# Kernel tuning notes

Hardware: AMD Instinct MI355X
Metric: run time of the kernel (lower is better)

The kernel has to match this reference:

```python
import jax, jax.numpy as jnp
import numpy as np

B, L, D = 4, 2048, 1024
H, DH = 16, 64  # heads, head dim (D = H*DH)


def setup_inputs() -> dict:
    key = jax.random.key(0)
    k1, k2, k3 = jax.random.split(key, 3)
    scale = D ** -0.5
    xin = jax.random.normal(k1, (B, L, D), dtype=jnp.float32)
    W_qkv = jax.random.normal(k2, (D, 3 * D), dtype=jnp.float32) * scale
    W_o = jax.random.normal(k3, (D, D), dtype=jnp.float32) * scale
    return {"xin": xin, "W_qkv": W_qkv, "W_o": W_o}


def reference(xin, W_qkv, W_o):
    b, Lq, _ = xin.shape
    # QKV projection: (b, L, 3D). NOTE: original torch code reshapes the
    # (b, L, 3D) buffer directly to (b, 3, H, L, DH) — a non-standard axis
    # interleave — which we replicate faithfully.
    QKV = (xin @ W_qkv).reshape(b, 3, H, Lq, DH)
    Q, K, V = QKV[:, 0], QKV[:, 1], QKV[:, 2]  # each (b, H, L, DH)
    scores = jnp.einsum("bhqd,bhkd->bhqk", Q, K) * (DH ** -0.5)
    attn = jax.nn.softmax(scores, axis=-1)  # dropout_prob=0.0 -> identity
    out = jnp.einsum("bhqk,bhkd->bhqd", attn, V)
    out = out.transpose(0, 2, 1, 3).reshape(b, Lq, H * DH)
    return out @ W_o
```

## Files before the change

### kernel.cpp

```cpp
#include <hip/hip_runtime.h>
#include <stdint.h>

typedef short short8 __attribute__((ext_vector_type(8)));
typedef float f32x4 __attribute__((ext_vector_type(4)));

#define LOG2E 1.44269504088896f
#define AS1 __attribute__((address_space(1)))
#define AS3 __attribute__((address_space(3)))

__device__ __forceinline__ float bfbits2f(unsigned short b) {
    unsigned u = ((unsigned)b) << 16;
    return __builtin_bit_cast(float, u);
}
__device__ __forceinline__ unsigned short f2bfbits(float f) {
    unsigned x = __builtin_bit_cast(unsigned, f);
    unsigned r = x + 0x7fffu + ((x >> 16) & 1u);
    return (unsigned short)(r >> 16);
}
__device__ __forceinline__ void unpack8(uint4 u, float4& f0, float4& f1) {
    f0.x = bfbits2f((unsigned short)(u.x & 0xffffu)); f0.y = bfbits2f((unsigned short)(u.x >> 16));
    f0.z = bfbits2f((unsigned short)(u.y & 0xffffu)); f0.w = bfbits2f((unsigned short)(u.y >> 16));
    f1.x = bfbits2f((unsigned short)(u.z & 0xffffu)); f1.y = bfbits2f((unsigned short)(u.z >> 16));
    f1.z = bfbits2f((unsigned short)(u.w & 0xffffu)); f1.w = bfbits2f((unsigned short)(u.w >> 16));
}
__device__ __forceinline__ unsigned pack2(float a, float b) {
    return (unsigned)f2bfbits(a) | ((unsigned)f2bfbits(b) << 16);
}
__device__ __forceinline__ float rsum16(float x) {
    x += __builtin_bit_cast(float, __builtin_amdgcn_mov_dpp(__builtin_bit_cast(int, x), 0x128, 0xf, 0xf, true));
    x += __builtin_bit_cast(float, __builtin_amdgcn_mov_dpp(__builtin_bit_cast(int, x), 0x124, 0xf, 0xf, true));
    x += __builtin_bit_cast(float, __builtin_amdgcn_mov_dpp(__builtin_bit_cast(int, x), 0x122, 0xf, 0xf, true));
    x += __builtin_bit_cast(float, __builtin_amdgcn_mov_dpp(__builtin_bit_cast(int, x), 0x121, 0xf, 0xf, true));
    return x;
}
__device__ __forceinline__ void glds16(const void* gp, void* lp) {
    __builtin_amdgcn_global_load_lds((const AS1 unsigned*)(uintptr_t)gp,
                                     (AS3 unsigned*)(unsigned)(uintptr_t)lp, 16, 0, 0);
}

__global__ __launch_bounds__(256) void xbf_k(const float* __restrict__ x,
                                             unsigned short* __restrict__ y) {
    int i = (blockIdx.x * 256 + threadIdx.x) * 4;
    float4 v = *(const float4*)(x + i);
    uint2 u;
    u.x = pack2(v.x, v.y);
    u.y = pack2(v.z, v.w);
    *(uint2*)(y + i) = u;
}

__global__ __launch_bounds__(256) void t32cvt_k(const float* __restrict__ src,
                                                unsigned short* __restrict__ dst,
                                                int R, int C) {
    __shared__ float tile[32][36];
    int t = threadIdx.x;
    int bx = blockIdx.x, by = blockIdx.y;
    int r = t >> 3, c0 = (t & 7) * 4;
    *(float4*)&tile[r][c0] = *(const float4*)(src + (size_t)(by * 32 + r) * C + bx * 32 + c0);
    __syncthreads();
    uint2 u;
    u.x = pack2(tile[c0 + 0][r], tile[c0 + 1][r]);
    u.y = pack2(tile[c0 + 2][r], tile[c0 + 3][r]);
    *(uint2*)(dst + (size_t)(bx * 32 + r) * R + by * 32 + c0) = u;
}

template <bool CF32>
__global__ __launch_bounds__(256) void gemm_k(const unsigned short* __restrict__ A,
                                              const unsigned short* __restrict__ Bt,
                                              void* __restrict__ Cv,
                                              int M, int N, int K) {
    __shared__ unsigned short sA[128 * 32];
    __shared__ unsigned short sB[128 * 32];
    int t = threadIdx.x;
    int wid = t >> 6, lane = t & 63;
    int wm = (wid >> 1) * 64, wn = (wid & 1) * 64;
    int lm = lane & 15, lq = lane >> 4;
    size_t m0 = (size_t)blockIdx.y * 128, n0 = (size_t)blockIdx.x * 128;
    int srow = t >> 2, scol = (t & 3) * 8;
    const unsigned short* ga0 = A + (m0 + srow) * K + scol;
    const unsigned short* ga1 = A + (m0 + 64 + srow) * K + scol;
    const unsigned short* gb0 = Bt + (n0 + srow) * K + scol;
    const unsigned short* gb1 = Bt + (n0 + 64 + srow) * K + scol;
    unsigned short* laA0 = &sA[wid * 512];
    unsigned short* laA1 = &sA[2048 + wid * 512];
    unsigned short* laB0 = &sB[wid * 512];
    unsigned short* laB1 = &sB[2048 + wid * 512];
    f32x4 acc[4][4] = {};
    for (int k0 = 0; k0 < K; k0 += 32) {
        __syncthreads();
        glds16(ga0 + k0, laA0);
        glds16(ga1 + k0, laA1);
        glds16(gb0 + k0, laB0);
        glds16(gb1 + k0, laB1);
        __syncthreads();
        short8 af[4], bfr[4];
        #pragma unroll
        for (int i = 0; i < 4; ++i) af[i] = *(const short8*)&sA[(wm + i * 16 + lm) * 32 + lq * 8];
        #pragma unroll
        for (int j = 0; j < 4; ++j) bfr[j] = *(const short8*)&sB[(wn + j * 16 + lm) * 32 + lq * 8];
        #pragma unroll
        for (int i = 0; i < 4; ++i)
            #pragma unroll
            for (int j = 0; j < 4; ++j)
                acc[i][j] = __builtin_amdgcn_mfma_f32_16x16x32_bf16(af[i], bfr[j], acc[i][j], 0, 0, 0);
    }
    #pragma unroll
    for (int i = 0; i < 4; ++i)
        #pragma unroll
        for (int j = 0; j < 4; ++j)
            #pragma unroll
            for (int r = 0; r < 4; ++r) {
                size_t row = m0 + wm + i * 16 + lq * 4 + r;
                size_t col = n0 + wn + j * 16 + lm;
                if (CF32) ((float*)Cv)[row * N + col] = acc[i][j][r];
                else ((unsigned short*)Cv)[row * N + col] = f2bfbits(acc[i][j][r]);
            }
}

__global__ __launch_bounds__(256) void vt_k(const unsigned short* __restrict__ qkv,
                                            unsigned short* __restrict__ vt) {
    __shared__ unsigned short tile[64 * 72];
    int kt = blockIdx.x, bh = blockIdx.y;
    int b = bh >> 4, h = bh & 15;
    const unsigned short* Vp = qkv + (size_t)b * 6291456 + 4194304 + (size_t)h * 131072;
    int t = threadIdx.x;
    int row = t >> 2, cc = (t & 3) * 16;
    const unsigned short* src = Vp + (size_t)(kt * 64 + row) * 64 + cc;
    *(uint4*)&tile[row * 72 + cc] = *(const uint4*)src;
    *(uint4*)&tile[row * 72 + cc + 8] = *(const uint4*)(src + 8);
    __syncthreads();
    unsigned v[8];
    #pragma unroll
    for (int j = 0; j < 8; ++j) {
        unsigned short a = tile[(cc + 2 * j) * 72 + row];
        unsigned short bsh = tile[(cc + 2 * j + 1) * 72 + row];
        v[j] = (unsigned)a | ((unsigned)bsh << 16);
    }
    unsigned short* dst = vt + ((size_t)bh * 64 + row) * 2048 + kt * 64 + cc;
    *(uint4*)dst = make_uint4(v[0], v[1], v[2], v[3]);
    *(uint4*)(dst + 8) = make_uint4(v[4], v[5], v[6], v[7]);
}

__global__ __launch_bounds__(256, 4) void attn_mfma(const unsigned short* __restrict__ qkv,
                                                    const unsigned short* __restrict__ vt,
                                                    unsigned short* __restrict__ aout) {
    __shared__ unsigned short Ks[64 * 72];
    __shared__ unsigned short Vs[64 * 72];
    __shared__ unsigned short Ps[4 * 32 * 72];
    int bid = blockIdx.x;
    int qt = bid & 15, h = (bid >> 4) & 15, b = bid >> 8;
    int t = threadIdx.x;
    int wave = t >> 6, lane = t & 63, lm = lane & 15, quad = lane >> 4;
    const unsigned short* Qb = qkv + (size_t)b * 6291456 + (size_t)h * 131072;
    const unsigned short* Kb = Qb + 2097152;
    const unsigned short* Vtb = vt + (size_t)(b * 16 + h) * 131072;
    int q0 = qt * 128 + wave * 32;

    short8 qf[2][2];
    #pragma unroll
    for (int i = 0; i < 2; ++i)
        #pragma unroll
        for (int c = 0; c < 2; ++c) {
            uint4 u = *(const uint4*)(Qb + (size_t)(q0 + i * 16 + lm) * 64 + c * 32 + quad * 8);
            float4 f0, f1; unpack8(u, f0, f1);
            uint4 v;
            v.x = pack2(f0.x * 0.125f, f0.y * 0.125f);
            v.y = pack2(f0.z * 0.125f, f0.w * 0.125f);
            v.z = pack2(f1.x * 0.125f, f1.y * 0.125f);
            v.w = pack2(f1.z * 0.125f, f1.w * 0.125f);
            qf[i][c] = *(short8*)&v;
        }

    float l_r[2][4] = {};
    f32x4 o[2][4] = {};

    int srow = t >> 2, scol = (t & 3) * 16;
    unsigned short* psw = Ps + wave * 2304;

    for (int kt = 0; kt < 32; ++kt) {
        const unsigned short* kp = Kb + (size_t)(kt * 64 + srow) * 64 + scol;
        uint4 k0 = *(const uint4*)kp;
        uint4 k1 = *(const uint4*)(kp + 8);
        const unsigned short* vp = Vtb + (size_t)srow * 2048 + kt * 64 + scol;
        uint4 v0 = *(const uint4*)vp;
        uint4 v1 = *(const uint4*)(vp + 8);
        __syncthreads();
        *(uint4*)&Ks[srow * 72 + scol] = k0;
        *(uint4*)&Ks[srow * 72 + scol + 8] = k1;
        *(uint4*)&Vs[srow * 72 + scol] = v0;
        *(uint4*)&Vs[srow * 72 + scol + 8] = v1;
        __syncthreads();

        f32x4 sf[2][4] = {};
        #pragma unroll
        for (int j = 0; j < 4; ++j) {
            short8 kf0 = *(const short8*)&Ks[(j * 16 + lm) * 72 + quad * 8];
            short8 kf1 = *(const short8*)&Ks[(j * 16 + lm) * 72 + 32 + quad * 8];
            #pragma unroll
            for (int i = 0; i < 2; ++i) {
                sf[i][j] = __builtin_amdgcn_mfma_f32_16x16x32_bf16(qf[i][0], kf0, sf[i][j], 0, 0, 0);
                sf[i][j] = __builtin_amdgcn_mfma_f32_16x16x32_bf16(qf[i][1], kf1, sf[i][j], 0, 0, 0);
            }
        }
        #pragma unroll
        for (int i = 0; i < 2; ++i)
            #pragma unroll
            for (int r = 0; r < 4; ++r) {
                int prow = (i * 16 + quad * 4 + r) * 72;
                #pragma unroll
                for (int j = 0; j < 4; ++j) {
                    float p = exp2f(sf[i][j][r] * LOG2E);
                    l_r[i][r] += p;
                    unsigned bits = __builtin_bit_cast(unsigned, p) + 0x8000u;
                    psw[prow + j * 16 + lm] = (unsigned short)(bits >> 16);
                }
            }
        __syncthreads();

        #pragma unroll
        for (int c = 0; c < 2; ++c) {
            short8 pf0 = *(const short8*)&psw[(0 * 16 + lm) * 72 + c * 32 + quad * 8];
            short8 pf1 = *(const short8*)&psw[(1 * 16 + lm) * 72 + c * 32 + quad * 8];
            #pragma unroll
            for (int jd = 0; jd < 4; ++jd) {
                short8 vf = *(const short8*)&Vs[(jd * 16 + lm) * 72 + c * 32 + quad * 8];
                o[0][jd] = __builtin_amdgcn_mfma_f32_16x16x32_bf16(pf0, vf, o[0][jd], 0, 0, 0);
                o[1][jd] = __builtin_amdgcn_mfma_f32_16x16x32_bf16(pf1, vf, o[1][jd], 0, 0, 0);
            }
        }
    }
    #pragma unroll
    for (int i = 0; i < 2; ++i)
        #pragma unroll
        for (int r = 0; r < 4; ++r) {
            float inv = 1.f / rsum16(l_r[i][r]);
            int q = q0 + i * 16 + quad * 4 + r;
            size_t rowbase = ((size_t)b * 2048 + q) * 1024 + h * 64;
            #pragma unroll
            for (int jd = 0; jd < 4; ++jd)
                aout[rowbase + jd * 16 + lm] = f2bfbits(o[i][jd][r] * inv);
        }
}

extern "C" void kernel_launch(void* const* d_in, const int* in_sizes, int n_in,
                              void* d_out, int out_size, void* d_ws, size_t ws_size,
                              hipStream_t stream) {
    const float* xin  = (const float*)d_in[0];
    const float* wqkv = (const float*)d_in[1];
    const float* wo   = (const float*)d_in[2];
    float* out = (float*)d_out;

    char* ws = (char*)d_ws;
    unsigned short* qkv   = (unsigned short*)(ws);
    unsigned short* attn  = (unsigned short*)(ws + 50331648);
    unsigned short* wqkvT = (unsigned short*)(ws + 67108864);
    unsigned short* woT   = (unsigned short*)(ws + 73400320);
    unsigned short* vt    = (unsigned short*)(ws + 75497472);
    unsigned short* xb    = (unsigned short*)(ws + 92274688);

    dim3 blk(256);
    xbf_k<<<dim3(8192), blk, 0, stream>>>(xin, xb);
    t32cvt_k<<<dim3(3072 / 32, 1024 / 32), blk, 0, stream>>>(wqkv, wqkvT, 1024, 3072);
    t32cvt_k<<<dim3(1024 / 32, 1024 / 32), blk, 0, stream>>>(wo, woT, 1024, 1024);
    gemm_k<false><<<dim3(3072 / 128, 8192 / 128), blk, 0, stream>>>(xb, wqkvT, qkv, 8192, 3072, 1024);
    vt_k<<<dim3(32, 64), blk, 0, stream>>>(qkv, vt);
    attn_mfma<<<dim3(1024), blk, 0, stream>>>(qkv, vt, attn);
    gemm_k<true><<<dim3(1024 / 128, 8192 / 128), blk, 0, stream>>>(attn, woT, out, 8192, 1024, 1024);
}
```

Measured before the change: 319.6 us.

## Enlarge attention query tile per wave and compute row sums via MFMA

```diff
diff --git a/kernel.cpp b/kernel.cpp
--- a/kernel.cpp
+++ b/kernel.cpp
@@ -8,14 +8,21 @@
 #define AS1 __attribute__((address_space(1)))
 #define AS3 __attribute__((address_space(3)))
 
-__device__ __forceinline__ float bfbits2f(unsigned short b) {
-    unsigned u = ((unsigned)b) << 16;
-    return __builtin_bit_cast(float, u);
+__device__ __forceinline__ float fexp2(float x) {
+#if __has_builtin(__builtin_amdgcn_exp2f)
+    return __builtin_amdgcn_exp2f(x);
+#else
+    return exp2f(x);
+#endif
 }
 __device__ __forceinline__ unsigned short f2bfbits(float f) {
     unsigned x = __builtin_bit_cast(unsigned, f);
     unsigned r = x + 0x7fffu + ((x >> 16) & 1u);
     return (unsigned short)(r >> 16);
+}
+__device__ __forceinline__ float bfbits2f(unsigned short b) {
+    unsigned u = ((unsigned)b) << 16;
+    return __builtin_bit_cast(float, u);
 }
 __device__ __forceinline__ void unpack8(uint4 u, float4& f0, float4& f1) {
     f0.x = bfbits2f((unsigned short)(u.x & 0xffffu)); f0.y = bfbits2f((unsigned short)(u.x >> 16));
@@ -25,13 +32,6 @@
 }
 __device__ __forceinline__ unsigned pack2(float a, float b) {
     return (unsigned)f2bfbits(a) | ((unsigned)f2bfbits(b) << 16);
-}
-__device__ __forceinline__ float rsum16(float x) {
-    x += __builtin_bit_cast(float, __builtin_amdgcn_mov_dpp(__builtin_bit_cast(int, x), 0x128, 0xf, 0xf, true));
-    x += __builtin_bit_cast(float, __builtin_amdgcn_mov_dpp(__builtin_bit_cast(int, x), 0x124, 0xf, 0xf, true));
-    x += __builtin_bit_cast(float, __builtin_amdgcn_mov_dpp(__builtin_bit_cast(int, x), 0x122, 0xf, 0xf, true));
-    x += __builtin_bit_cast(float, __builtin_amdgcn_mov_dpp(__builtin_bit_cast(int, x), 0x121, 0xf, 0xf, true));
-    return x;
 }
 __device__ __forceinline__ void glds16(const void* gp, void* lp) {
     __builtin_amdgcn_global_load_lds((const AS1 unsigned*)(uintptr_t)gp,
@@ -140,41 +140,46 @@
     *(uint4*)(dst + 8) = make_uint4(v[4], v[5], v[6], v[7]);
 }
 
-__global__ __launch_bounds__(256, 4) void attn_mfma(const unsigned short* __restrict__ qkv,
+__global__ __launch_bounds__(256, 2) void attn_mfma(const unsigned short* __restrict__ qkv,
                                                     const unsigned short* __restrict__ vt,
                                                     unsigned short* __restrict__ aout) {
     __shared__ unsigned short Ks[64 * 72];
     __shared__ unsigned short Vs[64 * 72];
-    __shared__ unsigned short Ps[4 * 32 * 72];
+    __shared__ unsigned short Ps[4 * 64 * 72];
     int bid = blockIdx.x;
-    int qt = bid & 15, h = (bid >> 4) & 15, b = bid >> 8;
+    int qt = bid & 7, h = (bid >> 3) & 15, b = bid >> 7;
     int t = threadIdx.x;
     int wave = t >> 6, lane = t & 63, lm = lane & 15, quad = lane >> 4;
     const unsigned short* Qb = qkv + (size_t)b * 6291456 + (size_t)h * 131072;
     const unsigned short* Kb = Qb + 2097152;
     const unsigned short* Vtb = vt + (size_t)(b * 16 + h) * 131072;
-    int q0 = qt * 128 + wave * 32;
-
-    short8 qf[2][2];
-    #pragma unroll
-    for (int i = 0; i < 2; ++i)
+    int q0 = qt * 256 + wave * 64;
+
+    const float qs = 0.125f * LOG2E;
+    short8 qf[4][2];
+    #pragma unroll
+    for (int i = 0; i < 4; ++i)
         #pragma unroll
         for (int c = 0; c < 2; ++c) {
             uint4 u = *(const uint4*)(Qb + (size_t)(q0 + i * 16 + lm) * 64 + c * 32 + quad * 8);
             float4 f0, f1; unpack8(u, f0, f1);
             uint4 v;
-            v.x = pack2(f0.x * 0.125f, f0.y * 0.125f);
-            v.y = pack2(f0.z * 0.125f, f0.w * 0.125f);
-            v.z = pack2(f1.x * 0.125f, f1.y * 0.125f);
-            v.w = pack2(f1.z * 0.125f, f1.w * 0.125f);
+            v.x = pack2(f0.x * qs, f0.y * qs);
+            v.y = pack2(f0.z * qs, f0.w * qs);
+            v.z = pack2(f1.x * qs, f1.y * qs);
+            v.w = pack2(f1.z * qs, f1.w * qs);
             qf[i][c] = *(short8*)&v;
         }
 
-    float l_r[2][4] = {};
-    f32x4 o[2][4] = {};
+    short8 ones;
+    #pragma unroll
+    for (int z = 0; z < 8; ++z) ones[z] = (short)0x3F80;
+
+    f32x4 o[4][4] = {};
+    f32x4 l_acc[4] = {};
 
     int srow = t >> 2, scol = (t & 3) * 16;
-    unsigned short* psw = Ps + wave * 2304;
+    unsigned short* psw = Ps + wave * 4608;
 
     for (int kt = 0; kt < 32; ++kt) {
         const unsigned short* kp = Kb + (size_t)(kt * 64 + srow) * 64 + scol;
@@ -190,49 +195,51 @@
         *(uint4*)&Vs[srow * 72 + scol + 8] = v1;
         __syncthreads();
 
-        f32x4 sf[2][4] = {};
         #pragma unroll
         for (int j = 0; j < 4; ++j) {
             short8 kf0 = *(const short8*)&Ks[(j * 16 + lm) * 72 + quad * 8];
             short8 kf1 = *(const short8*)&Ks[(j * 16 + lm) * 72 + 32 + quad * 8];
-            #pragma unroll
-            for (int i = 0; i < 2; ++i) {
-                sf[i][j] = __builtin_amdgcn_mfma_f32_16x16x32_bf16(qf[i][0], kf0, sf[i][j], 0, 0, 0);
-                sf[i][j] = __builtin_amdgcn_mfma_f32_16x16x32_bf16(qf[i][1], kf1, sf[i][j], 0, 0, 0);
+            f32x4 sf[4];
+            #pragma unroll
+            for (int i = 0; i < 4; ++i) {
+                sf[i] = (f32x4){0.f, 0.f, 0.f, 0.f};
+                sf[i] = __builtin_amdgcn_mfma_f32_16x16x32_bf16(qf[i][0], kf0, sf[i], 0, 0, 0);
+                sf[i] = __builtin_amdgcn_mfma_f32_16x16x32_bf16(qf[i][1], kf1, sf[i], 0, 0, 0);
             }
-        }
-        #pragma unroll
-        for (int i = 0; i < 2; ++i)
-            #pragma unroll
-            for (int r = 0; r < 4; ++r) {
-                int prow = (i * 16 + quad * 4 + r) * 72;
+            #pragma unroll
+            for (int i = 0; i < 4; ++i)
                 #pragma unroll
-                for (int j = 0; j < 4; ++j) {
-                    float p = exp2f(sf[i][j][r] * LOG2E);
-                    l_r[i][r] += p;
-                    unsigned bits = __builtin_bit_cast(unsigned, p) + 0x8000u;
-                    psw[prow + j * 16 + lm] = (unsigned short)(bits >> 16);
+                for (int r = 0; r < 4; ++r) {
+                    float p = fexp2(sf[i][r]);
+                    unsigned bits = __builtin_bit_cast(unsigned, p);
+                    psw[(i * 16 + quad * 4 + r) * 72 + j * 16 + lm] = (unsigned short)(bits >> 16);
                 }
-            }
+        }
         __syncthreads();
 
         #pragma unroll
         for (int c = 0; c < 2; ++c) {
-            short8 pf0 = *(const short8*)&psw[(0 * 16 + lm) * 72 + c * 32 + quad * 8];
-            short8 pf1 = *(const short8*)&psw[(1 * 16 + lm) * 72 + c * 32 + quad * 8];
+            short8 pf[4];
+            #pragma unroll
+            for (int i = 0; i < 4; ++i)
+                pf[i] = *(const short8*)&psw[(i * 16 + lm) * 72 + c * 32 + quad * 8];
             #pragma unroll
             for (int jd = 0; jd < 4; ++jd) {
                 short8 vf = *(const short8*)&Vs[(jd * 16 + lm) * 72 + c * 32 + quad * 8];
-                o[0][jd] = __builtin_amdgcn_mfma_f32_16x16x32_bf16(pf0, vf, o[0][jd], 0, 0, 0);
-                o[1][jd] = __builtin_amdgcn_mfma_f32_16x16x32_bf16(pf1, vf, o[1][jd], 0, 0, 0);
+                #pragma unroll
+                for (int i = 0; i < 4; ++i)
+                    o[i][jd] = __builtin_amdgcn_mfma_f32_16x16x32_bf16(pf[i], vf, o[i][jd], 0, 0, 0);
             }
+            #pragma unroll
+            for (int i = 0; i < 4; ++i)
+                l_acc[i] = __builtin_amdgcn_mfma_f32_16x16x32_bf16(pf[i], ones, l_acc[i], 0, 0, 0);
         }
     }
     #pragma unroll
-    for (int i = 0; i < 2; ++i)
+    for (int i = 0; i < 4; ++i)
         #pragma unroll
         for (int r = 0; r < 4; ++r) {
-            float inv = 1.f / rsum16(l_r[i][r]);
+            float inv = 1.f / l_acc[i][r];
             int q = q0 + i * 16 + quad * 4 + r;
             size_t rowbase = ((size_t)b * 2048 + q) * 1024 + h * 64;
             #pragma unroll
@@ -263,6 +270,6 @@
     t32cvt_k<<<dim3(1024 / 32, 1024 / 32), blk, 0, stream>>>(wo, woT, 1024, 1024);
     gemm_k<false><<<dim3(3072 / 128, 8192 / 128), blk, 0, stream>>>(xb, wqkvT, qkv, 8192, 3072, 1024);
     vt_k<<<dim3(32, 64), blk, 0, stream>>>(qkv, vt);
-    attn_mfma<<<dim3(1024), blk, 0, stream>>>(qkv, vt, attn);
+    attn_mfma<<<dim3(512), blk, 0, stream>>>(qkv, vt, attn);
     gemm_k<true><<<dim3(1024 / 128, 8192 / 128), blk, 0, stream>>>(attn, woT, out, 8192, 1024, 1024);
 }
```

New measurement: 299.6 us. 6.3% less time.
